# Optimization experiments

Hardware: AMD Instinct MI355X
Metric: run time of the kernel (lower is better)

## Reference

```python
import jax, jax.numpy as jnp
import numpy as np
import math

B, NI, NU, D, H, MAXNB, T = 1024, 50000, 20000, 256, 4, 20, 1000


def _cosine_sqrt_ab():
    t = jnp.linspace(0.0, T, T + 1) / T
    ab = jnp.cos((t + 0.008) / 1.008 * math.pi / 2) ** 2
    ab = ab / ab[0]
    ab = ab[1:]
    return jnp.sqrt(ab), jnp.sqrt(1.0 - ab)


def _ln(x, g, b, eps=1e-5):
    m = jnp.mean(x, -1, keepdims=True)
    v = jnp.var(x, -1, keepdims=True)
    return (x - m) / jnp.sqrt(v + eps) * g + b


def _mha(q, k, v, wqkv, bqkv, wo, bo):
    # torch nn.MultiheadAttention (batch_first) with packed in_proj
    d = q.shape[-1]
    dh = d // H
    wq, wk, wv = jnp.split(wqkv, 3, axis=0)
    bq, bk, bv = jnp.split(bqkv, 3, axis=0)
    def heads(x, w, bb):
        y = x @ w.T + bb
        return y.reshape(x.shape[0], x.shape[1], H, dh).transpose(0, 2, 1, 3)
    qh, kh, vh = heads(q, wq, bq), heads(k, wk, bk), heads(v, wv, bv)
    att = jax.nn.softmax(jnp.einsum('bhqd,bhkd->bhqk', qh, kh) / math.sqrt(dh), axis=-1)
    o = jnp.einsum('bhqk,bhkd->bhqd', att, vh)
    o = o.transpose(0, 2, 1, 3).reshape(q.shape[0], q.shape[1], d)
    return o @ wo.T + bo


def setup_inputs() -> dict:
    key = jax.random.key(0)
    ks = iter(jax.random.split(key, 64))
    p = lambda shape, s=0.02: jax.random.normal(next(ks), shape, jnp.float32) * s
    inp = {}
    inp['x0'] = (jax.random.uniform(next(ks), (B, NI)) < 0.05).astype(jnp.float32)
    inp['user_ids'] = jax.random.randint(next(ks), (B,), 0, NU)
    inp['t'] = jax.random.randint(next(ks), (B,), 0, T)
    inp['noise'] = jax.random.normal(next(ks), (B, D), jnp.float32)
    inp['neighbor_idx'] = jax.random.randint(next(ks), (NU, MAXNB), 0, NI)
    inp['item_emb'] = p((NI, D), 0.01)
    inp['enc_w1'] = p((2 * D, NI), 0.01); inp['enc_b1'] = jnp.zeros((2 * D,))
    inp['enc_w2'] = p((D, 2 * D)); inp['enc_b2'] = jnp.zeros((D,))
    inp['dec_w1'] = p((2 * D, D)); inp['dec_b1'] = jnp.zeros((2 * D,))
    inp['dec_w2'] = p((NI, 2 * D)); inp['dec_b2'] = jnp.zeros((NI,))
    inp['up_w'] = p((D, D)); inp['up_b'] = jnp.zeros((D,))
    inp['ip_w'] = p((D, D)); inp['ip_b'] = jnp.zeros((D,))
    inp['te_w1'] = p((32, 1)); inp['te_b1'] = jnp.zeros((32,))
    inp['te_w2'] = p((D, 32)); inp['te_b2'] = jnp.zeros((D,))
    inp['ca_wqkv'] = p((3 * D, D)); inp['ca_bqkv'] = jnp.zeros((3 * D,))
    inp['ca_wo'] = p((D, D)); inp['ca_bo'] = jnp.zeros((D,))
    inp['sa_wqkv'] = p((3 * D, D)); inp['sa_bqkv'] = jnp.zeros((3 * D,))
    inp['sa_wo'] = p((D, D)); inp['sa_bo'] = jnp.zeros((D,))
    inp['n1_g'] = jnp.ones((D,)); inp['n1_b'] = jnp.zeros((D,))
    inp['n2_g'] = jnp.ones((D,)); inp['n2_b'] = jnp.zeros((D,))
    inp['ff_w1'] = p((2 * D, D)); inp['ff_b1'] = jnp.zeros((2 * D,))
    inp['ff_w2'] = p((D, 2 * D)); inp['ff_b2'] = jnp.zeros((D,))
    return inp


def reference(x0, user_ids, t, noise, neighbor_idx, item_emb,
              enc_w1, enc_b1, enc_w2, enc_b2, dec_w1, dec_b1, dec_w2, dec_b2,
              up_w, up_b, ip_w, ip_b, te_w1, te_b1, te_w2, te_b2,
              ca_wqkv, ca_bqkv, ca_wo, ca_bo, sa_wqkv, sa_bqkv, sa_wo, sa_bo,
              n1_g, n1_b, n2_g, n2_b, ff_w1, ff_b1, ff_w2, ff_b2):
    gelu = lambda x: jax.nn.gelu(x, approximate=False)
    # encoder: (B, NI) -> (B, D)
    z0 = gelu(x0 @ enc_w1.T + enc_b1) @ enc_w2.T + enc_b2
    sqrt_ab, sqrt_1ab = _cosine_sqrt_ab()
    z_t = sqrt_ab[t][:, None] * z0 + sqrt_1ab[t][:, None] * noise
    # vectorized padded neighbor gather: (B, MAXNB, D)
    nb = item_emb[neighbor_idx[user_ids]]
    t_norm = t.astype(jnp.float32) / T
    # denoiser
    q = (z_t @ up_w.T + up_b)[:, None, :]
    kv = nb @ ip_w.T + ip_b
    te = jax.nn.silu(t_norm[:, None] @ te_w1.T + te_b1) @ te_w2.T + te_b2
    q = q + te[:, None, :]
    ca = _mha(q, kv, kv, ca_wqkv, ca_bqkv, ca_wo, ca_bo)
    h = _ln(q + ca, n1_g, n1_b)[:, 0, :]
    sa = _mha(h[:, None], h[:, None], h[:, None], sa_wqkv, sa_bqkv, sa_wo, sa_bo)[:, 0, :]
    h = _ln(h + sa, n2_g, n2_b)
    z_pred = h + (gelu(h @ ff_w1.T + ff_b1) @ ff_w2.T + ff_b2)
    diff_loss = jnp.mean((z_pred - z0) ** 2)
    logits = gelu(z0 @ dec_w1.T + dec_b1) @ dec_w2.T + dec_b2
    recon = jnp.mean(jax.nn.softplus(logits) - logits * x0)
    return diff_loss + 0.1 * recon
```

## Files before the change

### kernel.cpp

```cpp
#include <hip/hip_runtime.h>
#include <math.h>

#define NI   50000
#define Tt   1000
#define KP   50176
#define MW   1568
#define NPAD 50048

typedef __bf16 bf16x8 __attribute__((ext_vector_type(8)));
typedef float  f32x4  __attribute__((ext_vector_type(4)));

__device__ __forceinline__ unsigned short f2bf(float f) {
  unsigned u = __float_as_uint(f);
  u += 0x7FFFu + ((u >> 16) & 1u);
  return (unsigned short)(u >> 16);
}
__device__ __forceinline__ float bf2f(unsigned short u) {
  return __uint_as_float(((unsigned)u) << 16);
}
__device__ __forceinline__ unsigned pack2(float a, float b) {
  return (unsigned)f2bf(a) | ((unsigned)f2bf(b) << 16);
}
__device__ __forceinline__ f32x4 mfma16(const unsigned short* a, const unsigned short* b, f32x4 c) {
  typedef unsigned short u16x8 __attribute__((ext_vector_type(8)));
  u16x8 av = *(const u16x8*)a;
  u16x8 bv = *(const u16x8*)b;
  return __builtin_amdgcn_mfma_f32_16x16x32_bf16(
      __builtin_bit_cast(bf16x8, av), __builtin_bit_cast(bf16x8, bv), c, 0, 0, 0);
}
__device__ __forceinline__ float gelu_f(float x) {
  return 0.5f * x * (1.f + erff(x * 0.70710678118654752f));
}

#define GLD16(gsrc, ldst) __builtin_amdgcn_global_load_lds( \
    (const __attribute__((address_space(1))) unsigned int*)(const void*)(gsrc), \
    (__attribute__((address_space(3))) unsigned int*)(void*)(ldst), 16, 0, 0)

__global__ __launch_bounds__(256) void bm_expand(
    const float* __restrict__ x0, unsigned int* __restrict__ xmask,
    unsigned short* __restrict__ x0b)
{
  __shared__ unsigned int nib[256];
  int r = blockIdx.x, tid = threadIdx.x;
  const float* row = x0 + (size_t)r * NI;
  unsigned short* orow = x0b + (size_t)r * KP;
  unsigned int* mrow = xmask + (size_t)r * MW;
  for (int pass = 0; pass < 49; ++pass) {
    int base = pass * 1024;
    int k = base + tid * 4;
    float4 v = make_float4(0.f, 0.f, 0.f, 0.f);
    if (k + 4 <= NI) v = *(const float4*)(row + k);
    ushort4 ob;
    ob.x = v.x != 0.f ? 0x3F80 : 0; ob.y = v.y != 0.f ? 0x3F80 : 0;
    ob.z = v.z != 0.f ? 0x3F80 : 0; ob.w = v.w != 0.f ? 0x3F80 : 0;
    *(ushort4*)(orow + k) = ob;
    unsigned n4 = (v.x != 0.f ? 1u : 0u) | (v.y != 0.f ? 2u : 0u) |
                  (v.z != 0.f ? 4u : 0u) | (v.w != 0.f ? 8u : 0u);
    nib[tid] = n4;
    __syncthreads();
    if (tid < 32) {
      unsigned wv = 0;
#pragma unroll
      for (int j = 0; j < 8; ++j) wv |= nib[tid * 8 + j] << (4 * j);
      mrow[(base >> 5) + tid] = wv;
    }
    __syncthreads();
  }
}

__global__ __launch_bounds__(256) void cvt_w1(const float* __restrict__ src,
                                              unsigned short* __restrict__ dst) {
  int c = blockIdx.x * 2048 + threadIdx.x * 8;
  if (c >= KP) return;
  int r = blockIdx.y;
  const float* s = src + (size_t)r * NI;
  uint4 o;
  if (c + 8 <= NI) {
    float4 a = *(const float4*)(s + c), b = *(const float4*)(s + c + 4);
    o.x = pack2(a.x, a.y); o.y = pack2(a.z, a.w);
    o.z = pack2(b.x, b.y); o.w = pack2(b.z, b.w);
  } else {
    float v[8];
#pragma unroll
    for (int i = 0; i < 8; ++i) v[i] = (c + i < NI) ? s[c + i] : 0.f;
    o.x = pack2(v[0], v[1]); o.y = pack2(v[2], v[3]);
    o.z = pack2(v[4], v[5]); o.w = pack2(v[6], v[7]);
  }
  *(uint4*)(dst + (size_t)r * KP + c) = o;
}

__global__ __launch_bounds__(256) void cvt_w2n(const float* __restrict__ src,
                                               unsigned short* __restrict__ dst) {
  size_t idx = ((size_t)blockIdx.x * 256 + threadIdx.x) * 8;
  float4 a = *(const float4*)(src + idx), b = *(const float4*)(src + idx + 4);
  uint4 o;
  o.x = pack2(a.x, a.y); o.y = pack2(a.z, a.w);
  o.z = pack2(b.x, b.y); o.w = pack2(b.z, b.w);
  *(uint4*)(dst + idx) = o;
}

__global__ __launch_bounds__(256) void cvt_many(
    const float* s0, const float* s1, const float* s2, const float* s3,
    const float* s4, const float* s5, const float* s6,
    unsigned short* d0, unsigned short* d1, unsigned short* d2, unsigned short* d3,
    unsigned short* d4, unsigned short* d5, unsigned short* d6)
{
  const float* srcs[7] = {s0, s1, s2, s3, s4, s5, s6};
  unsigned short* dsts[7] = {d0, d1, d2, d3, d4, d5, d6};
  const int ns[7] = {131072, 65536, 65536, 65536, 131072, 131072, 131072};
  int j = blockIdx.y;
  int i = (blockIdx.x * 256 + threadIdx.x) * 8;
  if (i >= ns[j]) return;
  float4 a = *(const float4*)(srcs[j] + i), b = *(const float4*)(srcs[j] + i + 4);
  uint4 o;
  o.x = pack2(a.x, a.y); o.y = pack2(a.z, a.w);
  o.z = pack2(b.x, b.y); o.w = pack2(b.z, b.w);
  *(uint4*)(dsts[j] + i) = o;
}

__global__ __launch_bounds__(256) void compose_k(
    const float* __restrict__ ca_wqkv, const float* __restrict__ ca_bqkv,
    const float* __restrict__ ip_w, const float* __restrict__ ip_b,
    const float* __restrict__ sa_wqkv, const float* __restrict__ sa_bqkv,
    const float* __restrict__ sa_wo, const float* __restrict__ sa_bo,
    unsigned short* __restrict__ Wkv, float* __restrict__ bkv,
    unsigned short* __restrict__ Wsa, float* __restrict__ bsa)
{
  int b = blockIdx.x, k = threadIdx.x;
  if (b < 512) {
    const float* wrow = ca_wqkv + (size_t)(256 + b) * 256;
    float s = 0.f;
    for (int c = 0; c < 256; ++c) s += wrow[c] * ip_w[c * 256 + k];
    Wkv[b * 256 + k] = f2bf(s);
    if (k == 0) {
      float sb = 0.f;
      for (int c = 0; c < 256; ++c) sb += wrow[c] * ip_b[c];
      bkv[b] = sb + ca_bqkv[256 + b];
    }
  } else {
    int i = b - 512;
    const float* worow = sa_wo + (size_t)i * 256;
    float s = 0.f;
    for (int c = 0; c < 256; ++c) s += worow[c] * sa_wqkv[(512 + c) * 256 + k];
    Wsa[i * 256 + k] = f2bf(s);
    if (k == 0) {
      float sb = 0.f;
      for (int c = 0; c < 256; ++c) sb += worow[c] * sa_bqkv[512 + c];
      bsa[i] = sb + sa_bo[i];
    }
  }
}

template<int T>
__global__ __launch_bounds__(256) void gemm128(
    const unsigned short* __restrict__ A, int lda,
    const unsigned short* __restrict__ Bw, int ldb,
    const float* __restrict__ bias, void* __restrict__ Cv, int ldc, int K,
    const unsigned int* __restrict__ xmask, float* __restrict__ loss, int Nvalid)
{
  __shared__ __align__(16) unsigned short As[128 * 32];
  __shared__ __align__(16) unsigned short Bs[128 * 32];
  __shared__ unsigned int msk[128][4];
  __shared__ float red[4];
  const int tid = threadIdx.x;
  const int m0 = blockIdx.x * 128, n0 = blockIdx.y * 128;
  const int kb = (T == 2) ? blockIdx.z * K : 0;
  const int w = tid >> 6, l = tid & 63;
  const int wm = (w >> 1) * 64, wn = (w & 1) * 64;
  const int fr = l & 15, fo = (l >> 4) * 8;
  const int s0 = tid, s1 = tid + 256;
  const int iters = K >> 5;
  f32x4 acc[4][4] = {};
  for (int it = 0; it < iters; ++it) {
    int k0 = kb + it * 32;
    __syncthreads();
    GLD16(A  + (size_t)(m0 + (s0 >> 2)) * lda + k0 + (s0 & 3) * 8, &As[s0 * 8]);
    GLD16(A  + (size_t)(m0 + (s1 >> 2)) * lda + k0 + (s1 & 3) * 8, &As[s1 * 8]);
    GLD16(Bw + (size_t)(n0 + (s0 >> 2)) * ldb + k0 + (s0 & 3) * 8, &Bs[s0 * 8]);
    GLD16(Bw + (size_t)(n0 + (s1 >> 2)) * ldb + k0 + (s1 & 3) * 8, &Bs[s1 * 8]);
    __syncthreads();
    const unsigned short *ap[4], *bp[4];
#pragma unroll
    for (int i = 0; i < 4; ++i) {
      ap[i] = &As[(wm + 16 * i + fr) * 32 + fo];
      bp[i] = &Bs[(wn + 16 * i + fr) * 32 + fo];
    }
#pragma unroll
    for (int i = 0; i < 4; ++i)
#pragma unroll
      for (int j = 0; j < 4; ++j)
        acc[i][j] = mfma16(ap[i], bp[j], acc[i][j]);
  }
  const int cr = (l >> 4) * 4, cc = l & 15;
  if (T == 0) {
    unsigned short* Cb = (unsigned short*)Cv;
#pragma unroll
    for (int j = 0; j < 4; ++j) {
      int n = n0 + wn + 16 * j + cc;
      float bv = bias[n];
#pragma unroll
      for (int i = 0; i < 4; ++i)
#pragma unroll
        for (int r = 0; r < 4; ++r) {
          int m = m0 + wm + 16 * i + cr + r;
          Cb[(size_t)m * ldc + n] = f2bf(acc[i][j][r] + bv);
        }
    }
  } else if (T == 2) {
    float* Cf = (float*)Cv;
#pragma unroll
    for (int i = 0; i < 4; ++i)
#pragma unroll
      for (int j = 0; j < 4; ++j) {
        int n = n0 + wn + 16 * j + cc;
#pragma unroll
        for (int r = 0; r < 4; ++r) {
          int m = m0 + wm + 16 * i + cr + r;
          atomicAdd(&Cf[(size_t)m * ldc + n], acc[i][j][r]);
        }
      }
  } else {
    {
      int row = tid >> 1, p = tid & 1;
      *(uint2*)&msk[row][p * 2] =
          *(const uint2*)(xmask + (size_t)(m0 + row) * MW + (n0 >> 5) + p * 2);
    }
    __syncthreads();
    float ts = 0.f;
#pragma unroll
    for (int j = 0; j < 4; ++j) {
      int nl = wn + 16 * j + cc;
      int n = n0 + nl;
      if (n < Nvalid) {
        float bv = bias[n];
#pragma unroll
        for (int i = 0; i < 4; ++i)
#pragma unroll
          for (int r = 0; r < 4; ++r) {
            int ml = wm + 16 * i + cr + r;
            float lg = acc[i][j][r] + bv;
            float sp = fmaxf(lg, 0.f) + __logf(1.f + __expf(-fabsf(lg)));
            unsigned word = msk[ml][nl >> 5];
            ts += sp - (((word >> (nl & 31)) & 1u) ? lg : 0.f);
          }
      }
    }
    for (int off = 32; off > 0; off >>= 1) ts += __shfl_xor(ts, off);
    if (l == 0) red[w] = ts;
    __syncthreads();
    if (tid == 0) atomicAdd(loss, red[0] + red[1] + red[2] + red[3]);
  }
}

template<int EPI>
__global__ __launch_bounds__(256) void gemm64(
    const unsigned short* __restrict__ A, int lda,
    const unsigned short* __restrict__ Bw, int ldb,
    const float* __restrict__ bias, void* __restrict__ Cv, int ldc, int K,
    const void* __restrict__ R0, const void* __restrict__ R1, const void* __restrict__ R2,
    void* __restrict__ W0, void* __restrict__ W1, float* __restrict__ loss)
{
  __shared__ __align__(16) unsigned short As[64 * 32];
  __shared__ __align__(16) unsigned short Bs[64 * 32];
  __shared__ float red[4];
  const int tid = threadIdx.x;
  const int m0 = blockIdx.x * 64, n0 = blockIdx.y * 64;
  const int w = tid >> 6, l = tid & 63;
  const int wm = (w >> 1) * 32, wn = (w & 1) * 32;
  const int fr = l & 15, fo = (l >> 4) * 8;
  const int srow = tid >> 2, scol = (tid & 3) * 8;
  f32x4 acc[2][2] = {};
  for (int k0 = 0; k0 < K; k0 += 32) {
    __syncthreads();
    GLD16(A  + (size_t)(m0 + srow) * lda + k0 + scol, &As[tid * 8]);
    GLD16(Bw + (size_t)(n0 + srow) * ldb + k0 + scol, &Bs[tid * 8]);
    __syncthreads();
    const unsigned short* ap0 = &As[(wm +      fr) * 32 + fo];
    const unsigned short* ap1 = &As[(wm + 16 + fr) * 32 + fo];
    const unsigned short* bp0 = &Bs[(wn +      fr) * 32 + fo];
    const unsigned short* bp1 = &Bs[(wn + 16 + fr) * 32 + fo];
    acc[0][0] = mfma16(ap0, bp0, acc[0][0]);
    acc[0][1] = mfma16(ap0, bp1, acc[0][1]);
    acc[1][0] = mfma16(ap1, bp0, acc[1][0]);
    acc[1][1] = mfma16(ap1, bp1, acc[1][1]);
  }
  const int cr = (l >> 4) * 4, cc = l & 15;
  float ts = 0.f;
#pragma unroll
  for (int i = 0; i < 2; ++i)
#pragma unroll
    for (int j = 0; j < 2; ++j) {
      int n = n0 + wn + 16 * j + cc;
      float bv = bias[n];
#pragma unroll
      for (int r = 0; r < 4; ++r) {
        int m = m0 + wm + 16 * i + cr + r;
        float v = acc[i][j][r] + bv;
        size_t idx = (size_t)m * ldc + n;
        if (EPI == 0) ((float*)Cv)[idx] = v;
        if (EPI == 1) ((unsigned short*)Cv)[idx] = f2bf(v);
        if (EPI == 2) ((unsigned short*)Cv)[idx] = f2bf(gelu_f(v));
        if (EPI == 3) {
          ((float*)Cv)[idx] = v;
          ((unsigned short*)W0)[idx] = f2bf(v);
          float zt = ((const float*)R1)[m] * v +
                     ((const float*)R2)[m] * ((const float*)R0)[idx];
          ((unsigned short*)W1)[idx] = f2bf(zt);
        }
        if (EPI == 4) {
          v += ((const float*)R0)[idx];
          ((unsigned short*)Cv)[idx] = f2bf(v);
        }
        if (EPI == 5) {
          v += bf2f(((const unsigned short*)R0)[idx]);
          float d = v - ((const float*)R1)[idx];
          ts += d * d;
        }
      }
    }
  if (EPI == 5) {
    for (int off = 32; off > 0; off >>= 1) ts += __shfl_xor(ts, off);
    if (l == 0) red[w] = ts;
    __syncthreads();
    if (tid == 0) atomicAdd(loss, red[0] + red[1] + red[2] + red[3]);
  }
}

__global__ __launch_bounds__(256) void h1_epi(const float* __restrict__ S,
                                              const float* __restrict__ b,
                                              unsigned short* __restrict__ H) {
  int i = blockIdx.x * 256 + threadIdx.x;
  H[i] = f2bf(gelu_f(S[i] + b[i & 511]));
}

__global__ __launch_bounds__(256) void prep_te(
    const int* __restrict__ t,
    const float* __restrict__ te_w1, const float* __restrict__ te_b1,
    const float* __restrict__ te_w2, const float* __restrict__ te_b2,
    float* __restrict__ te, float* __restrict__ sab, float* __restrict__ s1ab)
{
  __shared__ float sj[32];
  int b = blockIdx.x, d = threadIdx.x;
  int ti = t[b];
  float tn = (float)ti / (float)Tt;
  if (d < 32) {
    float a = tn * te_w1[d] + te_b1[d];
    sj[d] = a / (1.f + __expf(-a));
  }
  if (d == 0) {
    double tt = (double)(ti + 1) / (double)Tt;
    double c  = cos((tt + 0.008) / 1.008 * M_PI * 0.5);
    double c0 = cos((0.008) / 1.008 * M_PI * 0.5);
    double ab = (c * c) / (c0 * c0);
    sab[b]  = (float)sqrt(ab);
    s1ab[b] = (float)sqrt(1.0 - ab);
  }
  __syncthreads();
  float accv = te_b2[d];
#pragma unroll
  for (int j = 0; j < 32; ++j) accv += sj[j] * te_w2[d * 32 + j];
  te[(size_t)b * 256 + d] = accv;
}

__global__ __launch_bounds__(256) void gather_nb(
    const int* __restrict__ uid, const int* __restrict__ nidx,
    const float* __restrict__ emb, unsigned short* __restrict__ nb)
{
  int b = blockIdx.x, j = blockIdx.y, d = threadIdx.x;
  int idx = nidx[uid[b] * 20 + j];
  nb[((size_t)b * 20 + j) * 256 + d] = f2bf(emb[(size_t)idx * 256 + d]);
}

__global__ __launch_bounds__(256) void attn_k(
    const float* __restrict__ qh, const unsigned short* __restrict__ kvh,
    unsigned short* __restrict__ o)
{
  int b = blockIdx.x, tid = threadIdx.x;
  int h = tid >> 6, d = tid & 63;
  float qv = qh[(size_t)b * 256 + h * 64 + d];
  const unsigned short* kbase = kvh + (size_t)b * 20 * 512 + h * 64 + d;
  const unsigned short* vbase = kbase + 256;
  float s[20];
#pragma unroll
  for (int k = 0; k < 20; ++k) {
    float p = qv * bf2f(kbase[k * 512]);
    for (int off = 32; off > 0; off >>= 1) p += __shfl_xor(p, off);
    s[k] = p * 0.125f;
  }
  float mx = s[0];
#pragma unroll
  for (int k = 1; k < 20; ++k) mx = fmaxf(mx, s[k]);
  float sum = 0.f;
#pragma unroll
  for (int k = 0; k < 20; ++k) { s[k] = __expf(s[k] - mx); sum += s[k]; }
  float inv = 1.f / sum;
  float ov = 0.f;
#pragma unroll
  for (int k = 0; k < 20; ++k) ov += s[k] * bf2f(vbase[k * 512]);
  o[(size_t)b * 256 + h * 64 + d] = f2bf(ov * inv);
}

__global__ __launch_bounds__(256) void ln_k(
    const unsigned short* __restrict__ X, const unsigned short* __restrict__ Y,
    const float* __restrict__ g, const float* __restrict__ bb,
    unsigned short* __restrict__ out)
{
  __shared__ float rs[4], rs2[4];
  int b = blockIdx.x, d = threadIdx.x;
  size_t i = (size_t)b * 256 + d;
  float v = bf2f(X[i]) + bf2f(Y[i]);
  float s = v, s2 = v * v;
  for (int off = 32; off > 0; off >>= 1) { s += __shfl_xor(s, off); s2 += __shfl_xor(s2, off); }
  int w = d >> 6, l = d & 63;
  if (l == 0) { rs[w] = s; rs2[w] = s2; }
  __syncthreads();
  s  = rs[0] + rs[1] + rs[2] + rs[3];
  s2 = rs2[0] + rs2[1] + rs2[2] + rs2[3];
  float mean = s * (1.f / 256.f);
  float var  = s2 * (1.f / 256.f) - mean * mean;
  out[i] = f2bf((v - mean) * rsqrtf(var + 1e-5f) * g[d] + bb[d]);
}

__global__ void final_k(const float* __restrict__ scal, float* __restrict__ out) {
  out[0] = scal[0] * (1.f / (1024.f * 256.f)) + 0.1f * scal[1] * (1.f / (1024.f * 50000.f));
}

extern "C" void kernel_launch(void* const* d_in, const int* in_sizes, int n_in,
                              void* d_out, int out_size, void* d_ws, size_t ws_size,
                              hipStream_t stream) {
  const float* x0      = (const float*)d_in[0];
  const int*   uid     = (const int*)  d_in[1];
  const int*   t       = (const int*)  d_in[2];
  const float* noise   = (const float*)d_in[3];
  const int*   nidx    = (const int*)  d_in[4];
  const float* item_emb= (const float*)d_in[5];
  const float* enc_w1  = (const float*)d_in[6];
  const float* enc_b1  = (const float*)d_in[7];
  const float* enc_w2  = (const float*)d_in[8];
  const float* enc_b2  = (const float*)d_in[9];
  const float* dec_w1  = (const float*)d_in[10];
  const float* dec_b1  = (const float*)d_in[11];
  const float* dec_w2  = (const float*)d_in[12];
  const float* dec_b2  = (const float*)d_in[13];
  const float* up_w    = (const float*)d_in[14];
  const float* up_b    = (const float*)d_in[15];
  const float* ip_w    = (const float*)d_in[16];
  const float* ip_b    = (const float*)d_in[17];
  const float* te_w1   = (const float*)d_in[18];
  const float* te_b1   = (const float*)d_in[19];
  const float* te_w2   = (const float*)d_in[20];
  const float* te_b2   = (const float*)d_in[21];
  const float* ca_wqkv = (const float*)d_in[22];
  const float* ca_bqkv = (const float*)d_in[23];
  const float* ca_wo   = (const float*)d_in[24];
  const float* ca_bo   = (const float*)d_in[25];
  const float* sa_wqkv = (const float*)d_in[26];
  const float* sa_bqkv = (const float*)d_in[27];
  const float* sa_wo   = (const float*)d_in[28];
  const float* sa_bo   = (const float*)d_in[29];
  const float* n1_g    = (const float*)d_in[30];
  const float* n1_b    = (const float*)d_in[31];
  const float* n2_g    = (const float*)d_in[32];
  const float* n2_b    = (const float*)d_in[33];
  const float* ff_w1   = (const float*)d_in[34];
  const float* ff_b1   = (const float*)d_in[35];
  const float* ff_w2   = (const float*)d_in[36];
  const float* ff_b2   = (const float*)d_in[37];
  (void)in_sizes; (void)n_in; (void)out_size; (void)ws_size;

  float* ws   = (float*)d_ws;
  float* scal = ws;
  float* OUT  = ws + 4;
  float* sab  = OUT + 524288;
  float* s1ab = sab + 1024;
  float* te   = s1ab + 1024;
  float* qhf  = te + 262144;
  float* z0f  = qhf + 262144;
  float* bkv  = z0f + 262144;
  float* bsa  = bkv + 512;
  unsigned int* xmask = (unsigned int*)(bsa + 256);
  unsigned short* sh  = (unsigned short*)(xmask + 1024 * MW);
  unsigned short* x0b = sh;
  unsigned short* w2n = sh;
  unsigned short* w1b = x0b + (size_t)1024 * KP;
  unsigned short* nbb = w1b + (size_t)512 * KP;
  unsigned short* kvhb= nbb + 5242880;
  unsigned short* H1b = kvhb + 10485760;
  unsigned short* z0b = H1b + 524288;
  unsigned short* ztb = z0b + 262144;
  unsigned short* qpb = ztb + 262144;
  unsigned short* ob  = qpb + 262144;
  unsigned short* cab = ob  + 262144;
  unsigned short* hb  = cab + 262144;
  unsigned short* saob= hb  + 262144;
  unsigned short* h2b = saob+ 262144;
  unsigned short* f1b = h2b + 262144;
  unsigned short* Gb  = f1b + 524288;
  unsigned short* enc_w2b = Gb + 524288;
  unsigned short* up_wb   = enc_w2b + 131072;
  unsigned short* ca_wqb  = up_wb + 65536;
  unsigned short* ca_wob  = ca_wqb + 65536;
  unsigned short* ff_w1b  = ca_wob + 65536;
  unsigned short* ff_w2b  = ff_w1b + 131072;
  unsigned short* dec_w1b = ff_w2b + 131072;
  unsigned short* Wkv     = dec_w1b + 131072;
  unsigned short* Wsab    = Wkv + 131072;

  hipMemsetAsync(d_ws, 0, (size_t)(4 + 524288) * sizeof(float), stream);

  prep_te<<<1024, 256, 0, stream>>>(t, te_w1, te_b1, te_w2, te_b2, te, sab, s1ab);
  bm_expand<<<1024, 256, 0, stream>>>(x0, xmask, x0b);
  cvt_w1<<<dim3(25, 512), 256, 0, stream>>>(enc_w1, w1b);
  cvt_many<<<dim3(64, 7), 256, 0, stream>>>(enc_w2, up_w, ca_wqkv, ca_wo, ff_w1, ff_w2, dec_w1,
                                            enc_w2b, up_wb, ca_wqb, ca_wob, ff_w1b, ff_w2b, dec_w1b);
  compose_k<<<768, 256, 0, stream>>>(ca_wqkv, ca_bqkv, ip_w, ip_b,
                                     sa_wqkv, sa_bqkv, sa_wo, sa_bo,
                                     Wkv, bkv, Wsab, bsa);
  gather_nb<<<dim3(1024, 20), 256, 0, stream>>>(uid, nidx, item_emb, nbb);

  gemm128<2><<<dim3(8, 4, 16), 256, 0, stream>>>(
      x0b, KP, w1b, KP, nullptr, OUT, 512, 3136, nullptr, nullptr, 0);
  h1_epi<<<2048, 256, 0, stream>>>(OUT, enc_b1, H1b);

  cvt_w2n<<<12500, 256, 0, stream>>>(dec_w2, w2n);

  gemm64<3><<<dim3(16, 4), 256, 0, stream>>>(
      H1b, 512, enc_w2b, 512, enc_b2, z0f, 256, 512, noise, sab, s1ab, z0b, ztb, nullptr);

  gemm64<4><<<dim3(16, 4), 256, 0, stream>>>(
      ztb, 256, up_wb, 256, up_b, qpb, 256, 256, te, nullptr, nullptr, nullptr, nullptr, nullptr);
  gemm64<0><<<dim3(16, 4), 256, 0, stream>>>(
      qpb, 256, ca_wqb, 256, ca_bqkv, qhf, 256, 256,
      nullptr, nullptr, nullptr, nullptr, nullptr, nullptr);

  gemm128<0><<<dim3(160, 4), 256, 0, stream>>>(
      nbb, 256, Wkv, 256, bkv, kvhb, 512, 256, nullptr, nullptr, 0);

  attn_k<<<1024, 256, 0, stream>>>(qhf, kvhb, ob);
  gemm64<1><<<dim3(16, 4), 256, 0, stream>>>(
      ob, 256, ca_wob, 256, ca_bo, cab, 256, 256,
      nullptr, nullptr, nullptr, nullptr, nullptr, nullptr);
  ln_k<<<1024, 256, 0, stream>>>(qpb, cab, n1_g, n1_b, hb);

  gemm64<1><<<dim3(16, 4), 256, 0, stream>>>(
      hb, 256, Wsab, 256, bsa, saob, 256, 256,
      nullptr, nullptr, nullptr, nullptr, nullptr, nullptr);
  ln_k<<<1024, 256, 0, stream>>>(hb, saob, n2_g, n2_b, h2b);

  gemm64<2><<<dim3(16, 8), 256, 0, stream>>>(
      h2b, 256, ff_w1b, 256, ff_b1, f1b, 512, 256,
      nullptr, nullptr, nullptr, nullptr, nullptr, nullptr);
  gemm64<5><<<dim3(16, 4), 256, 0, stream>>>(
      f1b, 512, ff_w2b, 512, ff_b2, nullptr, 256, 512,
      h2b, z0f, nullptr, nullptr, nullptr, &scal[0]);

  gemm64<2><<<dim3(16, 8), 256, 0, stream>>>(
      z0b, 256, dec_w1b, 256, dec_b1, Gb, 512, 256,
      nullptr, nullptr, nullptr, nullptr, nullptr, nullptr);
  gemm128<1><<<dim3(8, 391), 256, 0, stream>>>(
      Gb, 512, w2n, 512, dec_b2, nullptr, 0, 512, xmask, &scal[1], NI);

  final_k<<<1, 1, 0, stream>>>(scal, (float*)d_out);
}
```

Baseline: 962.9 us.

## Swizzle GEMM block order, replace split-K atomics with partial buffers, parallelize bitmask expand

The encoder split-K GEMM now writes each K-chunk to its own fp32 partial buffer instead of using atomicAdd, and h1_epi sums the 16 partials. This removes atomic contention and the large workspace memset, at the cost of extra memory traffic for the partials. The encoder and decoder GEMMs use a 1D grid with a grouped block order so neighbouring blocks share A/B tiles in cache. bm_expand is split across a 2D grid with 8 elements per thread instead of a serial 49-pass loop per row, and the workspace layout and launch order are shuffled so the partials alias the later gather buffers.

```diff
diff --git a/kernel.cpp b/kernel.cpp
--- a/kernel.cpp
+++ b/kernel.cpp
@@ -41,30 +41,33 @@
     unsigned short* __restrict__ x0b)
 {
   __shared__ unsigned int nib[256];
-  int r = blockIdx.x, tid = threadIdx.x;
+  int r = blockIdx.y, tid = threadIdx.x;
+  int c0 = blockIdx.x * 2048;
+  int k = c0 + tid * 8;
   const float* row = x0 + (size_t)r * NI;
-  unsigned short* orow = x0b + (size_t)r * KP;
-  unsigned int* mrow = xmask + (size_t)r * MW;
-  for (int pass = 0; pass < 49; ++pass) {
-    int base = pass * 1024;
-    int k = base + tid * 4;
-    float4 v = make_float4(0.f, 0.f, 0.f, 0.f);
-    if (k + 4 <= NI) v = *(const float4*)(row + k);
-    ushort4 ob;
-    ob.x = v.x != 0.f ? 0x3F80 : 0; ob.y = v.y != 0.f ? 0x3F80 : 0;
-    ob.z = v.z != 0.f ? 0x3F80 : 0; ob.w = v.w != 0.f ? 0x3F80 : 0;
-    *(ushort4*)(orow + k) = ob;
-    unsigned n4 = (v.x != 0.f ? 1u : 0u) | (v.y != 0.f ? 2u : 0u) |
-                  (v.z != 0.f ? 4u : 0u) | (v.w != 0.f ? 8u : 0u);
-    nib[tid] = n4;
-    __syncthreads();
-    if (tid < 32) {
-      unsigned wv = 0;
-#pragma unroll
-      for (int j = 0; j < 8; ++j) wv |= nib[tid * 8 + j] << (4 * j);
-      mrow[(base >> 5) + tid] = wv;
-    }
-    __syncthreads();
+  float4 a = make_float4(0.f, 0.f, 0.f, 0.f), b = a;
+  if (k + 8 <= NI) {
+    a = *(const float4*)(row + k);
+    b = *(const float4*)(row + k + 4);
+  }
+  uint4 o;
+  o.x = (a.x != 0.f ? 0x3F80u : 0u) | (a.y != 0.f ? 0x3F800000u : 0u);
+  o.y = (a.z != 0.f ? 0x3F80u : 0u) | (a.w != 0.f ? 0x3F800000u : 0u);
+  o.z = (b.x != 0.f ? 0x3F80u : 0u) | (b.y != 0.f ? 0x3F800000u : 0u);
+  o.w = (b.z != 0.f ? 0x3F80u : 0u) | (b.w != 0.f ? 0x3F800000u : 0u);
+  if (k < KP) *(uint4*)(x0b + (size_t)r * KP + k) = o;
+  unsigned bits8 =
+      (a.x != 0.f ? 1u : 0u)  | (a.y != 0.f ? 2u : 0u)  |
+      (a.z != 0.f ? 4u : 0u)  | (a.w != 0.f ? 8u : 0u)  |
+      (b.x != 0.f ? 16u : 0u) | (b.y != 0.f ? 32u : 0u) |
+      (b.z != 0.f ? 64u : 0u) | (b.w != 0.f ? 128u : 0u);
+  nib[tid] = bits8;
+  __syncthreads();
+  if (tid < 64) {
+    unsigned wv = nib[tid * 4] | (nib[tid * 4 + 1] << 8) |
+                  (nib[tid * 4 + 2] << 16) | (nib[tid * 4 + 3] << 24);
+    int widx = (c0 >> 5) + tid;
+    if (widx < MW) xmask[(size_t)r * MW + widx] = wv;
   }
 }
 
@@ -163,13 +166,30 @@
   __shared__ unsigned int msk[128][4];
   __shared__ float red[4];
   const int tid = threadIdx.x;
-  const int m0 = blockIdx.x * 128, n0 = blockIdx.y * 128;
-  const int kb = (T == 2) ? blockIdx.z * K : 0;
+  int m0, n0, kb = 0, kc = 0, iters;
+  if (T == 2) {
+    int id = blockIdx.x;
+    int g = (id & 7) + 8 * (id >> 6);
+    m0 = ((id >> 3) & 7) * 128;
+    n0 = (g & 3) * 128;
+    kc = g >> 2;
+    kb = kc * 3136;
+    iters = 98;
+  } else if (T == 1) {
+    int id = blockIdx.x;
+    int n = (id & 7) + 8 * (id >> 6);
+    if (n >= 391) return;
+    m0 = ((id >> 3) & 7) * 128;
+    n0 = n * 128;
+    iters = 16;
+  } else {
+    m0 = blockIdx.x * 128; n0 = blockIdx.y * 128;
+    iters = K >> 5;
+  }
   const int w = tid >> 6, l = tid & 63;
   const int wm = (w >> 1) * 64, wn = (w & 1) * 64;
   const int fr = l & 15, fo = (l >> 4) * 8;
   const int s0 = tid, s1 = tid + 256;
-  const int iters = K >> 5;
   f32x4 acc[4][4] = {};
   for (int it = 0; it < iters; ++it) {
     int k0 = kb + it * 32;
@@ -207,7 +227,7 @@
         }
     }
   } else if (T == 2) {
-    float* Cf = (float*)Cv;
+    float* Cp = (float*)Cv + (size_t)kc * 524288;
 #pragma unroll
     for (int i = 0; i < 4; ++i)
 #pragma unroll
@@ -216,7 +236,7 @@
 #pragma unroll
         for (int r = 0; r < 4; ++r) {
           int m = m0 + wm + 16 * i + cr + r;
-          atomicAdd(&Cf[(size_t)m * ldc + n], acc[i][j][r]);
+          Cp[(size_t)m * 512 + n] = acc[i][j][r];
         }
       }
   } else {
@@ -326,11 +346,14 @@
   }
 }
 
-__global__ __launch_bounds__(256) void h1_epi(const float* __restrict__ S,
+__global__ __launch_bounds__(256) void h1_epi(const float* __restrict__ P,
                                               const float* __restrict__ b,
                                               unsigned short* __restrict__ H) {
   int i = blockIdx.x * 256 + threadIdx.x;
-  H[i] = f2bf(gelu_f(S[i] + b[i & 511]));
+  float s = b[i & 511];
+#pragma unroll
+  for (int k = 0; k < 16; ++k) s += P[(size_t)k * 524288 + i];
+  H[i] = f2bf(gelu_f(s));
 }
 
 __global__ __launch_bounds__(256) void prep_te(
@@ -470,8 +493,7 @@
 
   float* ws   = (float*)d_ws;
   float* scal = ws;
-  float* OUT  = ws + 4;
-  float* sab  = OUT + 524288;
+  float* sab  = ws + 4;
   float* s1ab = sab + 1024;
   float* te   = s1ab + 1024;
   float* qhf  = te + 262144;
@@ -480,23 +502,24 @@
   float* bsa  = bkv + 512;
   unsigned int* xmask = (unsigned int*)(bsa + 256);
   unsigned short* sh  = (unsigned short*)(xmask + 1024 * MW);
-  unsigned short* x0b = sh;
-  unsigned short* w2n = sh;
-  unsigned short* w1b = x0b + (size_t)1024 * KP;
-  unsigned short* nbb = w1b + (size_t)512 * KP;
-  unsigned short* kvhb= nbb + 5242880;
-  unsigned short* H1b = kvhb + 10485760;
-  unsigned short* z0b = H1b + 524288;
-  unsigned short* ztb = z0b + 262144;
-  unsigned short* qpb = ztb + 262144;
-  unsigned short* ob  = qpb + 262144;
-  unsigned short* cab = ob  + 262144;
-  unsigned short* hb  = cab + 262144;
-  unsigned short* saob= hb  + 262144;
-  unsigned short* h2b = saob+ 262144;
-  unsigned short* f1b = h2b + 262144;
-  unsigned short* Gb  = f1b + 524288;
-  unsigned short* enc_w2b = Gb + 524288;
+  float*          OUTp = (float*)sh;
+  unsigned short* nbb  = sh;
+  unsigned short* kvhb = nbb + 5242880;
+  unsigned short* f1b  = kvhb + 10485760;
+  unsigned short* Gb   = f1b + 524288;
+  unsigned short* x0b  = Gb + 524288;
+  unsigned short* w2n  = x0b;
+  unsigned short* w1b  = x0b + (size_t)1024 * KP;
+  unsigned short* H1b  = w1b + (size_t)512 * KP;
+  unsigned short* z0b  = H1b + 524288;
+  unsigned short* ztb  = z0b + 262144;
+  unsigned short* qpb  = ztb + 262144;
+  unsigned short* ob   = qpb + 262144;
+  unsigned short* cab  = ob  + 262144;
+  unsigned short* hb   = cab + 262144;
+  unsigned short* saob = hb  + 262144;
+  unsigned short* h2b  = saob+ 262144;
+  unsigned short* enc_w2b = h2b + 262144;
   unsigned short* up_wb   = enc_w2b + 131072;
   unsigned short* ca_wqb  = up_wb + 65536;
   unsigned short* ca_wob  = ca_wqb + 65536;
@@ -506,23 +529,26 @@
   unsigned short* Wkv     = dec_w1b + 131072;
   unsigned short* Wsab    = Wkv + 131072;
 
-  hipMemsetAsync(d_ws, 0, (size_t)(4 + 524288) * sizeof(float), stream);
+  hipMemsetAsync(scal, 0, 4 * sizeof(float), stream);
 
   prep_te<<<1024, 256, 0, stream>>>(t, te_w1, te_b1, te_w2, te_b2, te, sab, s1ab);
-  bm_expand<<<1024, 256, 0, stream>>>(x0, xmask, x0b);
+  bm_expand<<<dim3(25, 1024), 256, 0, stream>>>(x0, xmask, x0b);
   cvt_w1<<<dim3(25, 512), 256, 0, stream>>>(enc_w1, w1b);
   cvt_many<<<dim3(64, 7), 256, 0, stream>>>(enc_w2, up_w, ca_wqkv, ca_wo, ff_w1, ff_w2, dec_w1,
                                             enc_w2b, up_wb, ca_wqb, ca_wob, ff_w1b, ff_w2b, dec_w1b);
   compose_k<<<768, 256, 0, stream>>>(ca_wqkv, ca_bqkv, ip_w, ip_b,
                                      sa_wqkv, sa_bqkv, sa_wo, sa_bo,
                                      Wkv, bkv, Wsab, bsa);
+
+  gemm128<2><<<512, 256, 0, stream>>>(
+      x0b, KP, w1b, KP, nullptr, OUTp, 512, 3136, nullptr, nullptr, 0);
+  h1_epi<<<2048, 256, 0, stream>>>(OUTp, enc_b1, H1b);
+
+  cvt_w2n<<<12500, 256, 0, stream>>>(dec_w2, w2n);
+
   gather_nb<<<dim3(1024, 20), 256, 0, stream>>>(uid, nidx, item_emb, nbb);
-
-  gemm128<2><<<dim3(8, 4, 16), 256, 0, stream>>>(
-      x0b, KP, w1b, KP, nullptr, OUT, 512, 3136, nullptr, nullptr, 0);
-  h1_epi<<<2048, 256, 0, stream>>>(OUT, enc_b1, H1b);
-
-  cvt_w2n<<<12500, 256, 0, stream>>>(dec_w2, w2n);
+  gemm128<0><<<dim3(160, 4), 256, 0, stream>>>(
+      nbb, 256, Wkv, 256, bkv, kvhb, 512, 256, nullptr, nullptr, 0);
 
   gemm64<3><<<dim3(16, 4), 256, 0, stream>>>(
       H1b, 512, enc_w2b, 512, enc_b2, z0f, 256, 512, noise, sab, s1ab, z0b, ztb, nullptr);
@@ -532,9 +558,6 @@
   gemm64<0><<<dim3(16, 4), 256, 0, stream>>>(
       qpb, 256, ca_wqb, 256, ca_bqkv, qhf, 256, 256,
       nullptr, nullptr, nullptr, nullptr, nullptr, nullptr);
-
-  gemm128<0><<<dim3(160, 4), 256, 0, stream>>>(
-      nbb, 256, Wkv, 256, bkv, kvhb, 512, 256, nullptr, nullptr, 0);
 
   attn_k<<<1024, 256, 0, stream>>>(qhf, kvhb, ob);
   gemm64<1><<<dim3(16, 4), 256, 0, stream>>>(
@@ -557,7 +580,7 @@
   gemm64<2><<<dim3(16, 8), 256, 0, stream>>>(
       z0b, 256, dec_w1b, 256, dec_b1, Gb, 512, 256,
       nullptr, nullptr, nullptr, nullptr, nullptr, nullptr);
-  gemm128<1><<<dim3(8, 391), 256, 0, stream>>>(
+  gemm128<1><<<3136, 256, 0, stream>>>(
       Gb, 512, w2n, 512, dec_b2, nullptr, 0, 512, xmask, &scal[1], NI);
 
   final_k<<<1, 1, 0, stream>>>(scal, (float*)d_out);
```

New measurement: 904.1 us. 6.1% less time.
